# Kernel optimization log

Hardware: AMD Instinct MI355X
Metric: run time of the kernel (lower is better)

The kernel has to match this reference:

```python
import jax, jax.numpy as jnp
import numpy as np

IN_CHANNELS = 128
KERNEL = 3

def setup_inputs() -> dict:
    key = jax.random.key(0)
    k1, k2, k3 = jax.random.split(key, 3)
    B, C, L = 32, IN_CHANNELS, 8192
    inputs = jax.random.normal(k1, (B, C, L), dtype=jnp.float32)
    # per-channel Conv1d(1,1,k=3) weights/biases; PyTorch init U(-1/sqrt(3), 1/sqrt(3))
    bound = 1.0 / np.sqrt(KERNEL)
    weight = jax.random.uniform(k2, (C, KERNEL), dtype=jnp.float32, minval=-bound, maxval=bound)
    bias = jax.random.uniform(k3, (C,), dtype=jnp.float32, minval=-bound, maxval=bound)
    return {"inputs": inputs, "weight": weight, "bias": bias}

def reference(inputs, weight, bias):
    # Depthwise conv1d, kernel=3, stride=1, padding=1 (cross-correlation like torch Conv1d).
    B, C, L = inputs.shape
    xp = jnp.pad(inputs, ((0, 0), (0, 0), (1, 1)))  # [B, C, L+2]
    # out[b,c,l] = sum_k weight[c,k] * xp[b,c,l+k] + bias[c]
    out = (weight[None, :, 0:1] * xp[:, :, 0:L]
           + weight[None, :, 1:2] * xp[:, :, 1:L + 1]
           + weight[None, :, 2:3] * xp[:, :, 2:L + 2]
           + bias[None, :, None])
    return out
```

## Files before the change

### kernel.cpp

```cpp
#include <hip/hip_runtime.h>


constexpr int C  = 128;
constexpr int L  = 8192;
constexpr int L4 = L / 4;
constexpr int B  = 32;
constexpr int TOTAL4 = B * C * L4;

__global__ __launch_bounds__(256) void dwconv1d_kernel(
    const float4* __restrict__ x4,
    const float* __restrict__ x,
    const float* __restrict__ w,
    const float* __restrict__ bias,
    float4* __restrict__ out4)
{
    int idx  = blockIdx.x * blockDim.x + threadIdx.x;
    int lane = threadIdx.x & 63;
    int i4   = idx & (L4 - 1);

    int c = __builtin_amdgcn_readfirstlane((idx >> 11) & (C - 1));
    float w0 = w[c * 3 + 0];
    float w1 = w[c * 3 + 1];
    float w2 = w[c * 3 + 2];
    float bc = bias[c];

    float4 v = x4[idx];

    float left  = __shfl_up(v.w, 1);
    float right = __shfl_down(v.x, 1);

    long base = (long)idx * 4;
    if (lane == 0)  left  = (i4 == 0)      ? 0.0f : x[base - 1];
    if (lane == 63) right = (i4 == L4 - 1) ? 0.0f : x[base + 4];

    float4 o;
    o.x = fmaf(w0, left, fmaf(w1, v.x, fmaf(w2, v.y, bc)));
    o.y = fmaf(w0, v.x,  fmaf(w1, v.y, fmaf(w2, v.z, bc)));
    o.z = fmaf(w0, v.y,  fmaf(w1, v.z, fmaf(w2, v.w, bc)));
    o.w = fmaf(w0, v.z,  fmaf(w1, v.w, fmaf(w2, right, bc)));

    out4[idx] = o;
}

extern "C" void kernel_launch(void* const* d_in, const int* in_sizes, int n_in,
                              void* d_out, int out_size, void* d_ws, size_t ws_size,
                              hipStream_t stream)
{
    const float* x    = (const float*)d_in[0];
    const float* w    = (const float*)d_in[1];
    const float* bias = (const float*)d_in[2];
    float* out        = (float*)d_out;

    const int block = 256;
    const int grid  = TOTAL4 / block;

    dwconv1d_kernel<<<grid, block, 0, stream>>>(
        (const float4*)x, x, w, bias, (float4*)out);
}
```

Before: 224.4 us.

## Use persistent grid-stride loop with batched loads and nontemporal stores

Launches a fixed grid of 2048 blocks in which each thread processes 16 float4 elements, issuing 4 loads at a time before computing. The stride keeps each thread on the same channel, so the weights and bias are loaded once. Outputs are written with nontemporal stores to avoid polluting the cache. The aim is more bytes in flight per thread and less per-block overhead, at the cost of higher register use and possibly lower occupancy.

```diff
diff --git a/kernel.cpp b/kernel.cpp
--- a/kernel.cpp
+++ b/kernel.cpp
@@ -7,39 +7,70 @@
 constexpr int B  = 32;
 constexpr int TOTAL4 = B * C * L4;
 
-__global__ __launch_bounds__(256) void dwconv1d_kernel(
+constexpr int BLOCK  = 256;
+constexpr int GRID   = 2048;
+constexpr int STRIDE = BLOCK * GRID;
+constexpr int ITER   = TOTAL4 / STRIDE;
+constexpr int BATCH  = 4;
+
+static_assert(TOTAL4 % STRIDE == 0, "exact tiling");
+static_assert((STRIDE / L4) % C == 0, "channel invariant across iterations");
+
+typedef float floatx4 __attribute__((ext_vector_type(4)));
+
+__global__ __launch_bounds__(BLOCK) void dwconv1d_kernel(
     const float4* __restrict__ x4,
     const float* __restrict__ x,
     const float* __restrict__ w,
     const float* __restrict__ bias,
     float4* __restrict__ out4)
 {
-    int idx  = blockIdx.x * blockDim.x + threadIdx.x;
-    int lane = threadIdx.x & 63;
-    int i4   = idx & (L4 - 1);
+    const int idx0 = blockIdx.x * BLOCK + threadIdx.x;
+    const int lane = threadIdx.x & 63;
+    const int i4   = idx0 & (L4 - 1);
 
-    int c = __builtin_amdgcn_readfirstlane((idx >> 11) & (C - 1));
-    float w0 = w[c * 3 + 0];
-    float w1 = w[c * 3 + 1];
-    float w2 = w[c * 3 + 2];
-    float bc = bias[c];
+    const int c = __builtin_amdgcn_readfirstlane((idx0 >> 11) & (C - 1));
+    const float w0 = w[c * 3 + 0];
+    const float w1 = w[c * 3 + 1];
+    const float w2 = w[c * 3 + 2];
+    const float bc = bias[c];
 
-    float4 v = x4[idx];
+    const bool lane0    = (lane == 0);
+    const bool lane63   = (lane == 63);
+    const bool rowstart = (i4 == 0);
+    const bool rowend   = (i4 == L4 - 1);
 
-    float left  = __shfl_up(v.w, 1);
-    float right = __shfl_down(v.x, 1);
+    #pragma unroll
+    for (int jo = 0; jo < ITER / BATCH; ++jo) {
+        int    idx[BATCH];
+        float4 v[BATCH];
 
-    long base = (long)idx * 4;
-    if (lane == 0)  left  = (i4 == 0)      ? 0.0f : x[base - 1];
-    if (lane == 63) right = (i4 == L4 - 1) ? 0.0f : x[base + 4];
+        #pragma unroll
+        for (int ji = 0; ji < BATCH; ++ji) {
+            idx[ji] = idx0 + (jo * BATCH + ji) * STRIDE;
+            v[ji]   = x4[idx[ji]];
+        }
 
-    float4 o;
-    o.x = fmaf(w0, left, fmaf(w1, v.x, fmaf(w2, v.y, bc)));
-    o.y = fmaf(w0, v.x,  fmaf(w1, v.y, fmaf(w2, v.z, bc)));
-    o.z = fmaf(w0, v.y,  fmaf(w1, v.z, fmaf(w2, v.w, bc)));
-    o.w = fmaf(w0, v.z,  fmaf(w1, v.w, fmaf(w2, right, bc)));
+        #pragma unroll
+        for (int ji = 0; ji < BATCH; ++ji) {
+            const float4 vv = v[ji];
 
-    out4[idx] = o;
+            float left  = __shfl_up(vv.w, 1);
+            float right = __shfl_down(vv.x, 1);
+
+            const long base = (long)idx[ji] * 4;
+            if (lane0)  left  = rowstart ? 0.0f : x[base - 1];
+            if (lane63) right = rowend   ? 0.0f : x[base + 4];
+
+            floatx4 o;
+            o.x = fmaf(w0, left,  fmaf(w1, vv.x, fmaf(w2, vv.y, bc)));
+            o.y = fmaf(w0, vv.x,  fmaf(w1, vv.y, fmaf(w2, vv.z, bc)));
+            o.z = fmaf(w0, vv.y,  fmaf(w1, vv.z, fmaf(w2, vv.w, bc)));
+            o.w = fmaf(w0, vv.z,  fmaf(w1, vv.w, fmaf(w2, right, bc)));
+
+            __builtin_nontemporal_store(o, (floatx4*)&out4[idx[ji]]);
+        }
+    }
 }
 
 extern "C" void kernel_launch(void* const* d_in, const int* in_sizes, int n_in,
@@ -51,9 +82,6 @@
     const float* bias = (const float*)d_in[2];
     float* out        = (float*)d_out;
 
-    const int block = 256;
-    const int grid  = TOTAL4 / block;
-
-    dwconv1d_kernel<<<grid, block, 0, stream>>>(
+    dwconv1d_kernel<<<GRID, BLOCK, 0, stream>>>(
         (const float4*)x, x, w, bias, (float4*)out);
 }
```

After: 237.1 us. +5.7%, slower.
